# Optimization experiments

Hardware: AMD Instinct MI355X
Metric: run time of the kernel (lower is better)

## Reference

```python
import jax, jax.numpy as jnp
import numpy as np
from jax import lax

B, T, D_IN, D_H, D_OUT = 64, 512, 256, 1024, 256


def setup_inputs() -> dict:
    key = jax.random.key(0)
    k1, k2, k3, k4 = jax.random.split(key, 4)
    # lecun_normal-style scaling: std = 1/sqrt(fan_in)
    inputs = jax.random.normal(k1, (B, T, D_IN), dtype=jnp.float32)
    input_kernel = jax.random.normal(k2, (D_IN, D_H), dtype=jnp.float32) / np.sqrt(D_IN)
    hidden_kernel = jax.random.normal(k3, (D_H, D_H), dtype=jnp.float32) / np.sqrt(D_H)
    hidden_bias = jnp.zeros((D_H,), dtype=jnp.float32)
    output_kernel = jax.random.normal(k4, (D_H, D_OUT), dtype=jnp.float32) / np.sqrt(D_H)
    output_bias = jnp.zeros((D_OUT,), dtype=jnp.float32)
    return {
        "inputs": inputs,
        "input_kernel": input_kernel,
        "hidden_kernel": hidden_kernel,
        "hidden_bias": hidden_bias,
        "output_kernel": output_kernel,
        "output_bias": output_bias,
    }


def reference(inputs, input_kernel, hidden_kernel, hidden_bias, output_kernel, output_bias):
    # inputs: [B, T, D_in]. Precompute the input projection for all timesteps
    # (batched GEMM) — same math as per-step x_t @ W_in inside scan.
    x_proj = jnp.einsum("bti,ih->bth", inputs, input_kernel) + hidden_bias  # [B,T,H]
    x_proj_tm = jnp.swapaxes(x_proj, 0, 1)  # time-major [T,B,H]

    def step(h, xp_t):
        h_new = jnp.tanh(xp_t + jnp.dot(h, hidden_kernel))  # [B,H]
        return h_new, h_new

    h0 = jnp.zeros((inputs.shape[0], hidden_kernel.shape[0]), dtype=inputs.dtype)
    _, hidden_states = lax.scan(step, h0, x_proj_tm)  # [T,B,H]
    hidden_states = jnp.swapaxes(hidden_states, 0, 1)  # [B,T,H]
    # Dense readout applied to every timestep (return_sequences=True)
    outputs = jnp.einsum("bth,ho->bto", hidden_states, output_kernel) + output_bias
    return outputs
```

## Files before the change

### kernel.cpp

```cpp
#include <hip/hip_runtime.h>
#include <stdint.h>
#include <stddef.h>


#define TT 512
#define HH 1024

typedef __attribute__((ext_vector_type(8))) short short8;
typedef __attribute__((ext_vector_type(4))) float f32x4;
typedef unsigned long long u64;

#define POISON 0xAAAAAAAAAAAAAAAAull

__device__ inline short f2bf(float f) {
  uint32_t u = __builtin_bit_cast(uint32_t, f);
  u += 0x7fffu + ((u >> 16) & 1u);
  return (short)(u >> 16);
}

__device__ inline float fast_tanh(float x) {
  float ax = fabsf(x);
  float e = __expf(-2.f * ax);
  float r = (1.f - e) * __builtin_amdgcn_rcpf(1.f + e);
  return copysignf(r, x);
}

__global__ __launch_bounds__(256, 1) void xproj_kernel(
    const float* __restrict__ inp,
    const float* __restrict__ w_in,
    const float* __restrict__ h_b,
    float* __restrict__ xp) {
  const int blk = blockIdx.x;
  const int c = blk & 3, s = blk >> 2;
  const int tid = threadIdx.x;
  const int wv = tid >> 6, l = tid & 63, lr = l & 15, lq = l >> 4;

  __shared__ short ldsA[16 * 264];

  short8 wf[8][4];
#pragma unroll
  for (int kt = 0; kt < 8; ++kt)
#pragma unroll
    for (int nt = 0; nt < 4; ++nt) {
      int col = c * 256 + (wv * 4 + nt) * 16 + lr;
      int k0 = kt * 32 + lq * 8;
      short8 v;
#pragma unroll
      for (int e = 0; e < 8; ++e) v[e] = f2bf(w_in[(size_t)(k0 + e) * HH + col]);
      wf[kt][nt] = v;
    }
  float bias[4];
#pragma unroll
  for (int nt = 0; nt < 4; ++nt) bias[nt] = h_b[c * 256 + (wv * 4 + nt) * 16 + lr];

  for (int it = 0; it < 32; ++it) {
    int m = s + 64 * it;
    int t = m >> 2, g = m & 3;
    {
      int row = tid >> 4, cb = (tid & 15) * 16;
      const float* src = inp + ((size_t)(g * 16 + row) * TT + t) * 256 + cb;
      f32x4 v0 = *(const f32x4*)(src);
      f32x4 v1 = *(const f32x4*)(src + 4);
      f32x4 v2 = *(const f32x4*)(src + 8);
      f32x4 v3 = *(const f32x4*)(src + 12);
      short8 sa, sb;
      sa[0]=f2bf(v0[0]); sa[1]=f2bf(v0[1]); sa[2]=f2bf(v0[2]); sa[3]=f2bf(v0[3]);
      sa[4]=f2bf(v1[0]); sa[5]=f2bf(v1[1]); sa[6]=f2bf(v1[2]); sa[7]=f2bf(v1[3]);
      sb[0]=f2bf(v2[0]); sb[1]=f2bf(v2[1]); sb[2]=f2bf(v2[2]); sb[3]=f2bf(v2[3]);
      sb[4]=f2bf(v3[0]); sb[5]=f2bf(v3[1]); sb[6]=f2bf(v3[2]); sb[7]=f2bf(v3[3]);
      *(short8*)&ldsA[row * 264 + cb] = sa;
      *(short8*)&ldsA[row * 264 + cb + 8] = sb;
    }
    __syncthreads();

    f32x4 acc[4];
#pragma unroll
    for (int nt = 0; nt < 4; ++nt) acc[nt] = (f32x4){0.f, 0.f, 0.f, 0.f};
#pragma unroll
    for (int kt = 0; kt < 8; ++kt) {
      short8 a = *(const short8*)&ldsA[lr * 264 + kt * 32 + lq * 8];
#pragma unroll
      for (int nt = 0; nt < 4; ++nt)
        acc[nt] = __builtin_amdgcn_mfma_f32_16x16x32_bf16(a, wf[kt][nt], acc[nt], 0, 0, 0);
    }
#pragma unroll
    for (int nt = 0; nt < 4; ++nt) {
      f32x4 o;
#pragma unroll
      for (int i2 = 0; i2 < 4; ++i2) o[i2] = acc[nt][i2] + bias[nt];
      *(f32x4*)(xp + ((size_t)(t * 4 + g) * 64 + c * 16 + wv * 4 + nt) * 256 + l * 4) = o;
    }
    __syncthreads();
  }
}

__global__ __launch_bounds__(256, 1) void scan_kernel(
    const float* __restrict__ xp, const float* __restrict__ w_h,
    short* __restrict__ hbuf) {
  const int blk = blockIdx.x;
  const int g = blk & 3, j = blk >> 2;
  const int tid = threadIdx.x;
  const int wv = tid >> 6, l = tid & 63, lr = l & 15, lq = l >> 4;
  const int ntg = j * 4 + wv;

  __shared__ f32x4 red[4][4][64];
  __shared__ short tr[16][72];

  short8 wf[8][4];
#pragma unroll
  for (int f = 0; f < 8; ++f)
#pragma unroll
    for (int nt = 0; nt < 4; ++nt) {
      int n = j * 64 + nt * 16 + lr;
      int k0 = wv * 256 + f * 32 + lq * 8;
      short8 v;
#pragma unroll
      for (int e = 0; e < 8; ++e) v[e] = f2bf(w_h[(size_t)(k0 + e) * HH + n]);
      wf[f][nt] = v;
    }

  const u64* hq = (const u64*)hbuf;
  u64* hqw = (u64*)hbuf;

  for (int t = 0; t < TT; ++t) {
    f32x4 xpv = *(const f32x4*)(xp + ((size_t)(t * 4 + g) * 64 + ntg) * 256 + l * 4);

    f32x4 acc[4];
#pragma unroll
    for (int nt = 0; nt < 4; ++nt) acc[nt] = (f32x4){0.f, 0.f, 0.f, 0.f};

    if (t > 0) {
      u64 q[16];
      size_t base = (((size_t)((t - 1) * 4 + g) * 32 + wv * 8) * 64 + l) * 2;
      int bad;
      do {
#pragma unroll
        for (int f = 0; f < 8; ++f) {
          q[2 * f]     = __hip_atomic_load(hq + base + (size_t)f * 128,
                                           __ATOMIC_RELAXED, __HIP_MEMORY_SCOPE_AGENT);
          q[2 * f + 1] = __hip_atomic_load(hq + base + (size_t)f * 128 + 1,
                                           __ATOMIC_RELAXED, __HIP_MEMORY_SCOPE_AGENT);
        }
        int mybad = 0;
#pragma unroll
        for (int i = 0; i < 16; ++i) mybad |= (q[i] == POISON);
        bad = __any(mybad);
      } while (bad);

      short8 af[8];
#pragma unroll
      for (int f = 0; f < 8; ++f) {
        union { u64 qq[2]; short8 s; } u;
        u.qq[0] = q[2 * f];
        u.qq[1] = q[2 * f + 1];
        af[f] = u.s;
      }
#pragma unroll
      for (int f = 0; f < 8; ++f)
#pragma unroll
        for (int nt = 0; nt < 4; ++nt)
          acc[nt] = __builtin_amdgcn_mfma_f32_16x16x32_bf16(af[f], wf[f][nt], acc[nt], 0, 0, 0);
    }

    red[wv][0][l] = acc[0];
    red[wv][1][l] = acc[1];
    red[wv][2][l] = acc[2];
    red[wv][3][l] = acc[3];
    __syncthreads();
    f32x4 tot = red[0][wv][l] + red[1][wv][l] + red[2][wv][l] + red[3][wv][l];

#pragma unroll
    for (int i2 = 0; i2 < 4; ++i2) {
      float v = tot[i2] + xpv[i2];
      tr[lq * 4 + i2][wv * 16 + lr] = f2bf(fast_tanh(v));
    }
    __syncthreads();

    if (wv < 2) {
      short8 hv = *(const short8*)&tr[lr][wv * 32 + lq * 8];
      union { short8 s; u64 qq[2]; } u;
      u.s = hv;
      size_t wbase = (((size_t)(t * 4 + g) * 32 + (j * 2 + wv)) * 64 + l) * 2;
      __hip_atomic_store(hqw + wbase, u.qq[0],
                         __ATOMIC_RELAXED, __HIP_MEMORY_SCOPE_AGENT);
      __hip_atomic_store(hqw + wbase + 1, u.qq[1],
                         __ATOMIC_RELAXED, __HIP_MEMORY_SCOPE_AGENT);
    }
  }
}

__global__ __launch_bounds__(256, 1) void outproj_kernel(
    const short* __restrict__ hbuf, const float* __restrict__ w_o,
    const float* __restrict__ o_b, float* __restrict__ out) {
  const int blk = blockIdx.x;
  const int c = blk & 3, s = blk >> 2;
  const int tid = threadIdx.x;
  const int wv = tid >> 6, l = tid & 63, lr = l & 15, lq = l >> 4;

  __shared__ f32x4 red[4][4][64];

  short8 wf[8][4];
#pragma unroll
  for (int f = 0; f < 8; ++f)
#pragma unroll
    for (int nt = 0; nt < 4; ++nt) {
      int o = c * 64 + nt * 16 + lr;
      int k0 = wv * 256 + f * 32 + lq * 8;
      short8 v;
#pragma unroll
      for (int e = 0; e < 8; ++e) v[e] = f2bf(w_o[(size_t)(k0 + e) * 256 + o]);
      wf[f][nt] = v;
    }
  float bias = o_b[c * 64 + wv * 16 + lr];
  const short8* hfr = (const short8*)hbuf;

  for (int it = 0; it < 32; ++it) {
    int m = s + 64 * it;
    int t = m >> 2, g = m & 3;
    short8 af[8];
    size_t base = ((size_t)(t * 4 + g) * 32 + wv * 8) * 64 + l;
#pragma unroll
    for (int f = 0; f < 8; ++f) af[f] = hfr[base + (size_t)f * 64];
    f32x4 acc[4];
#pragma unroll
    for (int nt = 0; nt < 4; ++nt) acc[nt] = (f32x4){0.f, 0.f, 0.f, 0.f};
#pragma unroll
    for (int f = 0; f < 8; ++f)
#pragma unroll
      for (int nt = 0; nt < 4; ++nt)
        acc[nt] = __builtin_amdgcn_mfma_f32_16x16x32_bf16(af[f], wf[f][nt], acc[nt], 0, 0, 0);

    red[wv][0][l] = acc[0];
    red[wv][1][l] = acc[1];
    red[wv][2][l] = acc[2];
    red[wv][3][l] = acc[3];
    __syncthreads();
    f32x4 tot = red[0][wv][l] + red[1][wv][l] + red[2][wv][l] + red[3][wv][l];
#pragma unroll
    for (int i2 = 0; i2 < 4; ++i2) {
      int b = g * 16 + lq * 4 + i2;
      out[((size_t)b * TT + t) * 256 + c * 64 + wv * 16 + lr] = tot[i2] + bias;
    }
    __syncthreads();
  }
}

extern "C" void kernel_launch(void* const* d_in, const int* in_sizes, int n_in,
                              void* d_out, int out_size, void* d_ws, size_t ws_size,
                              hipStream_t stream) {
  const float* inp  = (const float*)d_in[0];
  const float* w_in = (const float*)d_in[1];
  const float* w_h  = (const float*)d_in[2];
  const float* h_b  = (const float*)d_in[3];
  const float* w_o  = (const float*)d_in[4];
  const float* o_b  = (const float*)d_in[5];

  float* xp   = (float*)d_ws;
  short* hbuf = (short*)((char*)d_ws + (size_t)134217728);

  xproj_kernel<<<256, 256, 0, stream>>>(inp, w_in, h_b, xp);
  scan_kernel<<<64, 256, 0, stream>>>(xp, w_h, hbuf);
  outproj_kernel<<<256, 256, 0, stream>>>(hbuf, w_o, o_b, (float*)d_out);
}
```

Before: 1.385 ms.

## Remove second barrier in scan step and widen projection kernel grids

The scan kernel's per-step reduction now double-buffers the shared reduction array by timestep parity. Each wave keeps its own partial in registers and transposes its 16x16 tanh tile in a private LDS slab, then publishes it directly. This removes the second __syncthreads per step on the serial critical path. The xproj and outproj kernels are launched with 1024 blocks, each doing 8 iterations instead of 32, which adds parallelism but repeats the per-block weight conversion four times as often. Stores now use atomic exchange, and the hbuf write mapping is reorganised per wave.

```diff
diff --git a/kernel.cpp b/kernel.cpp
--- a/kernel.cpp
+++ b/kernel.cpp
@@ -53,8 +53,8 @@
 #pragma unroll
   for (int nt = 0; nt < 4; ++nt) bias[nt] = h_b[c * 256 + (wv * 4 + nt) * 16 + lr];
 
-  for (int it = 0; it < 32; ++it) {
-    int m = s + 64 * it;
+  for (int it = 0; it < 8; ++it) {
+    int m = s + 256 * it;
     int t = m >> 2, g = m & 3;
     {
       int row = tid >> 4, cb = (tid & 15) * 16;
@@ -103,8 +103,8 @@
   const int wv = tid >> 6, l = tid & 63, lr = l & 15, lq = l >> 4;
   const int ntg = j * 4 + wv;
 
-  __shared__ f32x4 red[4][4][64];
-  __shared__ short tr[16][72];
+  __shared__ f32x4 red[2][4][4][64];
+  __shared__ short ldsw[4][16 * 24];
 
   short8 wf[8][4];
 #pragma unroll
@@ -162,29 +162,37 @@
           acc[nt] = __builtin_amdgcn_mfma_f32_16x16x32_bf16(af[f], wf[f][nt], acc[nt], 0, 0, 0);
     }
 
-    red[wv][0][l] = acc[0];
-    red[wv][1][l] = acc[1];
-    red[wv][2][l] = acc[2];
-    red[wv][3][l] = acc[3];
-    __syncthreads();
-    f32x4 tot = red[0][wv][l] + red[1][wv][l] + red[2][wv][l] + red[3][wv][l];
-
+    const int bi = t & 1;
+    f32x4 own = acc[0];
+#pragma unroll
+    for (int nt = 0; nt < 4; ++nt) {
+      if (nt == wv) own = acc[nt];
+      else red[bi][wv][nt][l] = acc[nt];
+    }
+    __syncthreads();
+
+    f32x4 tot = own;
+#pragma unroll
+    for (int p = 0; p < 4; ++p)
+      if (p != wv) tot += red[bi][p][wv][l];
+
+    short* lw = &ldsw[wv][0];
 #pragma unroll
     for (int i2 = 0; i2 < 4; ++i2) {
       float v = tot[i2] + xpv[i2];
-      tr[lq * 4 + i2][wv * 16 + lr] = f2bf(fast_tanh(v));
-    }
-    __syncthreads();
-
-    if (wv < 2) {
-      short8 hv = *(const short8*)&tr[lr][wv * 32 + lq * 8];
+      lw[(lq * 4 + i2) * 24 + lr] = f2bf(fast_tanh(v));
+    }
+    if (l < 32) {
+      short8 hv = *(const short8*)&lw[(l & 15) * 24 + (l >> 4) * 8];
       union { short8 s; u64 qq[2]; } u;
       u.s = hv;
-      size_t wbase = (((size_t)(t * 4 + g) * 32 + (j * 2 + wv)) * 64 + l) * 2;
-      __hip_atomic_store(hqw + wbase, u.qq[0],
-                         __ATOMIC_RELAXED, __HIP_MEMORY_SCOPE_AGENT);
-      __hip_atomic_store(hqw + wbase + 1, u.qq[1],
-                         __ATOMIC_RELAXED, __HIP_MEMORY_SCOPE_AGENT);
+      const int kt = 2 * j + (wv >> 1);
+      size_t wb = ((size_t)(t * 4 + g) * 32 + kt) * 128 +
+                  ((size_t)(l + 32 * (wv & 1))) * 2;
+      (void)__hip_atomic_exchange(hqw + wb, u.qq[0],
+                                  __ATOMIC_RELAXED, __HIP_MEMORY_SCOPE_AGENT);
+      (void)__hip_atomic_exchange(hqw + wb + 1, u.qq[1],
+                                  __ATOMIC_RELAXED, __HIP_MEMORY_SCOPE_AGENT);
     }
   }
 }
@@ -214,8 +222,8 @@
   float bias = o_b[c * 64 + wv * 16 + lr];
   const short8* hfr = (const short8*)hbuf;
 
-  for (int it = 0; it < 32; ++it) {
-    int m = s + 64 * it;
+  for (int it = 0; it < 8; ++it) {
+    int m = s + 256 * it;
     int t = m >> 2, g = m & 3;
     short8 af[8];
     size_t base = ((size_t)(t * 4 + g) * 32 + wv * 8) * 64 + l;
@@ -258,7 +266,7 @@
   float* xp   = (float*)d_ws;
   short* hbuf = (short*)((char*)d_ws + (size_t)134217728);
 
-  xproj_kernel<<<256, 256, 0, stream>>>(inp, w_in, h_b, xp);
+  xproj_kernel<<<1024, 256, 0, stream>>>(inp, w_in, h_b, xp);
   scan_kernel<<<64, 256, 0, stream>>>(xp, w_h, hbuf);
-  outproj_kernel<<<256, 256, 0, stream>>>(hbuf, w_o, o_b, (float*)d_out);
-}
+  outproj_kernel<<<1024, 256, 0, stream>>>(hbuf, w_o, o_b, (float*)d_out);
+}
```

Result: slower. 1.454 ms (+5.0%).
